# Optimization experiments

Measured on AMD Instinct MI355X. Metric: run time of the kernel, lower is better.

The kernel has to match this reference:

```python
import jax, jax.numpy as jnp
import numpy as np

H = 128  # LSTM units

def setup_inputs() -> dict:
    key = jax.random.key(0)
    ks = jax.random.split(key, 4)
    B, T, F = 16384, 28, 28
    x = jax.random.normal(ks[0], (B, T, F), dtype=jnp.float32)
    W = jax.random.normal(ks[1], (F, 4 * H), dtype=jnp.float32) * (1.0 / np.sqrt(F))
    U = jax.random.normal(ks[2], (H, 4 * H), dtype=jnp.float32) * (1.0 / np.sqrt(H))
    b = jnp.zeros((4 * H,), dtype=jnp.float32)
    Wd = jax.random.normal(ks[3], (H, 10), dtype=jnp.float32) * (1.0 / np.sqrt(H))
    bd = jnp.zeros((10,), dtype=jnp.float32)
    return {"x": x, "W": W, "U": U, "b": b, "Wd": Wd, "bd": bd}

def reference(x, W, U, b, Wd, bd):
    B = x.shape[0]
    # Precompute input projection for all timesteps: [B, T, 4H]
    xW = jnp.einsum('btf,fg->btg', x, W) + b
    xW_t = jnp.swapaxes(xW, 0, 1)  # [T, B, 4H] for scan

    def step(carry, xw):
        h, c = carry
        z = xw + h @ U  # [B, 4H]
        i, f, g, o = jnp.split(z, 4, axis=-1)  # Keras gate order: i, f, c, o
        i = jax.nn.sigmoid(i)
        f = jax.nn.sigmoid(f)
        g = jax.nn.relu(g)          # activation='relu' on cell candidate
        o = jax.nn.sigmoid(o)
        c_new = f * c + i * g
        h_new = o * jax.nn.relu(c_new)  # activation='relu' on cell state
        return (h_new, c_new), None

    h0 = jnp.zeros((B, H), dtype=x.dtype)
    c0 = jnp.zeros((B, H), dtype=x.dtype)
    (h_final, _), _ = jax.lax.scan(step, (h0, c0), xW_t)
    logits = h_final @ Wd + bd
    return jax.nn.softmax(logits, axis=-1)
```

## Files before the change

kernel.cpp:

```cpp
#include <hip/hip_runtime.h>
#include <math.h>

constexpr int LH = 128;
constexpr int LG = 512;
constexpr int LT = 28;
constexpr int LF = 28;
constexpr int NS = 16;
constexpr int NTH = 512;
constexpr int NREC = 8 * 4 * 5;

typedef short bf16x8 __attribute__((ext_vector_type(8)));
typedef float f32x4  __attribute__((ext_vector_type(4)));

__device__ __forceinline__ unsigned short rne_bf16(float f) {
    unsigned u = __builtin_bit_cast(unsigned, f);
    u += 0x7FFFu + ((u >> 16) & 1u);
    return (unsigned short)(u >> 16);
}
__device__ __forceinline__ float bf16_to_f(unsigned short v) {
    return __builtin_bit_cast(float, (unsigned)v << 16);
}
__device__ __forceinline__ float fsigmoid(float v) {
    return __builtin_amdgcn_rcpf(1.0f + __expf(-v));
}

__device__ __forceinline__ int h_idx(int row, int g, int w2) {
    return row * LH + (((g ^ (row & 15)) << 3) + w2);
}

__global__ __launch_bounds__(256) void pack_frags(
    const float* __restrict__ W, const float* __restrict__ U,
    const float* __restrict__ b, unsigned short* __restrict__ ws)
{
    const int gid = blockIdx.x * 256 + threadIdx.x;
    if (gid >= NREC * 64) return;
    const int lane = gid & 63;
    const int rec  = gid >> 6;
    const int kk   = rec % 5;
    const int wti  = rec / 5;
    const int ti   = wti & 3;
    const int w    = wti >> 2;
    const int r16  = lane & 15;
    const int quad = lane >> 4;
    const int col  = 128 * ti + 16 * w + r16;

    unsigned short v[8];
#pragma unroll
    for (int e = 0; e < 8; ++e) {
        float f;
        if (kk < 4) {
            f = U[(kk * 32 + quad * 8 + e) * LG + col];
        } else {
            const int k = quad * 8 + e;
            f = (k < LF) ? W[k * LG + col] : (k == LF ? b[col] : 0.0f);
        }
        v[e] = rne_bf16(f);
    }
    unsigned short* dst = ws + (size_t)gid * 8;
#pragma unroll
    for (int e = 0; e < 8; ++e) dst[e] = v[e];
}

__global__ __launch_bounds__(NTH, 4) void lstm_mfma(
    const float* __restrict__ x,
    const bf16x8* __restrict__ frag,
    const float* __restrict__ Wd,
    const float* __restrict__ bd,
    float* __restrict__ out)
{
    __shared__ unsigned short xfrag[LT][4][16][8];
    __shared__ unsigned short h_sh[2][NS * LH];
    __shared__ bf16x8 wlds[8 * 4 * 64];
    __shared__ float logit_lds[NS][10];

    const int tid  = threadIdx.x;
    const int wave = tid >> 6;
    const int lane = tid & 63;
    const int r16  = lane & 15;
    const int quad = lane >> 4;
    const long s0  = (long)blockIdx.x * NS;

    bf16x8 Uf[4][4];
#pragma unroll
    for (int ti = 0; ti < 4; ++ti)
#pragma unroll
        for (int kk = 0; kk < 4; ++kk)
            Uf[ti][kk] = frag[((wave * 4 + ti) * 5 + kk) * 64 + lane];

    for (int i = tid; i < 8 * 4 * 64; i += NTH)
        wlds[i] = frag[((i >> 6) * 5 + 4) * 64 + (i & 63)];

    for (int i = tid; i < NS * LH; i += NTH) h_sh[0][i] = 0;

#pragma unroll 1
    for (int i = tid; i < LT * NS * 32; i += NTH) {
        const int fpad = i & 31;
        const int s    = (i >> 5) & 15;
        const int t    = i >> 9;
        float v;
        if (fpad < LF)       v = x[(s0 + s) * (LT * LF) + t * LF + fpad];
        else if (fpad == LF) v = 1.0f;
        else                 v = 0.0f;
        xfrag[t][fpad >> 3][s][fpad & 7] = rne_bf16(v);
    }

    float cre[4];
#pragma unroll
    for (int e = 0; e < 4; ++e) cre[e] = 0.0f;

    int cur = 0;
#pragma unroll 1
    for (int t = 0; t < LT; ++t) {
        __syncthreads();

        f32x4 acc[4];
#pragma unroll
        for (int ti = 0; ti < 4; ++ti)
            acc[ti] = f32x4{0.0f, 0.0f, 0.0f, 0.0f};

        {
            const bf16x8 xa = *reinterpret_cast<const bf16x8*>(
                &xfrag[t][quad][r16][0]);
#pragma unroll
            for (int ti = 0; ti < 4; ++ti) {
                const bf16x8 wf = wlds[(wave * 4 + ti) * 64 + lane];
                acc[ti] = __builtin_amdgcn_mfma_f32_16x16x32_bf16(
                    xa, wf, acc[ti], 0, 0, 0);
            }
        }

#pragma unroll
        for (int kk = 0; kk < 4; ++kk) {
            const bf16x8 h0 = *reinterpret_cast<const bf16x8*>(
                &h_sh[cur][h_idx(r16, kk * 4 + quad, 0)]);
#pragma unroll
            for (int ti = 0; ti < 4; ++ti)
                acc[ti] = __builtin_amdgcn_mfma_f32_16x16x32_bf16(
                    h0, Uf[ti][kk], acc[ti], 0, 0, 0);
        }

        const int gW = 2 * wave + (r16 >> 3);
        const int w2 = r16 & 7;
#pragma unroll
        for (int e = 0; e < 4; ++e) {
            const float ig = fsigmoid(acc[0][e]);
            const float fg = fsigmoid(acc[1][e]);
            const float gg = fmaxf(acc[2][e], 0.0f);
            const float og = fsigmoid(acc[3][e]);
            const float cn = fg * cre[e] + ig * gg;
            cre[e] = cn;
            const float hv = og * fmaxf(cn, 0.0f);
            h_sh[cur ^ 1][h_idx(quad * 4 + e, gW, w2)] = rne_bf16(hv);
        }
        cur ^= 1;
    }

    __syncthreads();

    if (tid < NS * 10) {
        const int s   = tid / 10;
        const int cls = tid - s * 10;
        float a = bd[cls];
        for (int k = 0; k < LH; ++k) {
            const float hv = bf16_to_f(
                h_sh[cur][s * LH + ((((k >> 3) ^ s) << 3) + (k & 7))]);
            a += hv * Wd[k * 10 + cls];
        }
        logit_lds[s][cls] = a;
    }
    __syncthreads();

    if (tid < NS) {
        const int s = tid;
        float m = logit_lds[s][0];
#pragma unroll
        for (int q = 1; q < 10; ++q) m = fmaxf(m, logit_lds[s][q]);
        float e[10], sum = 0.0f;
#pragma unroll
        for (int q = 0; q < 10; ++q) {
            e[q] = expf(logit_lds[s][q] - m);
            sum += e[q];
        }
        const float inv = __builtin_amdgcn_rcpf(sum);
#pragma unroll
        for (int q = 0; q < 10; ++q)
            out[(s0 + s) * 10 + q] = e[q] * inv;
    }
}

extern "C" void kernel_launch(void* const* d_in, const int* in_sizes, int n_in,
                              void* d_out, int out_size, void* d_ws, size_t ws_size,
                              hipStream_t stream) {
    const float* x  = (const float*)d_in[0];
    const float* W  = (const float*)d_in[1];
    const float* U  = (const float*)d_in[2];
    const float* b  = (const float*)d_in[3];
    const float* Wd = (const float*)d_in[4];
    const float* bd = (const float*)d_in[5];
    float* out = (float*)d_out;

    const int B = in_sizes[0] / (LT * LF);
    const int blocks = B / NS;

    pack_frags<<<(NREC * 64 + 255) / 256, 256, 0, stream>>>(
        W, U, b, (unsigned short*)d_ws);
    lstm_mfma<<<blocks, NTH, 0, stream>>>(
        x, (const bf16x8*)d_ws, Wd, bd, out);
}
```

Measured before the change: 108.3 us.

## Process 64 sequences per block with register-resident W fragments

Each block now handles 64 sequences instead of 16, so every wave loops over four 16-row tiles while reusing the same U and W fragments held in registers. The W fragments move from LDS into registers, which removes the per-step LDS reads for them. Occupancy is pinned to 2 waves per EU and bf16 conversion uses the HIP intrinsic. The intent is to amortise weight loads and barriers over more rows, at the cost of 4x fewer blocks and higher register and LDS use.

```diff
diff --git a/kernel.cpp b/kernel.cpp
--- a/kernel.cpp
+++ b/kernel.cpp
@@ -1,11 +1,12 @@
 #include <hip/hip_runtime.h>
+#include <hip/hip_bf16.h>
 #include <math.h>
 
 constexpr int LH = 128;
 constexpr int LG = 512;
 constexpr int LT = 28;
 constexpr int LF = 28;
-constexpr int NS = 16;
+constexpr int NS = 64;
 constexpr int NTH = 512;
 constexpr int NREC = 8 * 4 * 5;
 
@@ -16,6 +17,10 @@
     unsigned u = __builtin_bit_cast(unsigned, f);
     u += 0x7FFFu + ((u >> 16) & 1u);
     return (unsigned short)(u >> 16);
+}
+__device__ __forceinline__ unsigned short hw_bf16(float f) {
+    __hip_bfloat16 h = __float2bfloat16(f);
+    return __builtin_bit_cast(unsigned short, h);
 }
 __device__ __forceinline__ float bf16_to_f(unsigned short v) {
     return __builtin_bit_cast(float, (unsigned)v << 16);
@@ -61,16 +66,16 @@
     for (int e = 0; e < 8; ++e) dst[e] = v[e];
 }
 
-__global__ __launch_bounds__(NTH, 4) void lstm_mfma(
+__global__ __attribute__((amdgpu_waves_per_eu(2, 2))) __launch_bounds__(NTH)
+void lstm_mfma(
     const float* __restrict__ x,
     const bf16x8* __restrict__ frag,
     const float* __restrict__ Wd,
     const float* __restrict__ bd,
     float* __restrict__ out)
 {
-    __shared__ unsigned short xfrag[LT][4][16][8];
+    __shared__ unsigned short xfrag[LT][4][4][16][8];
     __shared__ unsigned short h_sh[2][NS * LH];
-    __shared__ bf16x8 wlds[8 * 4 * 64];
     __shared__ float logit_lds[NS][10];
 
     const int tid  = threadIdx.x;
@@ -81,89 +86,85 @@
     const long s0  = (long)blockIdx.x * NS;
 
     bf16x8 Uf[4][4];
-#pragma unroll
-    for (int ti = 0; ti < 4; ++ti)
+    bf16x8 Wf[4];
+#pragma unroll
+    for (int ti = 0; ti < 4; ++ti) {
 #pragma unroll
         for (int kk = 0; kk < 4; ++kk)
             Uf[ti][kk] = frag[((wave * 4 + ti) * 5 + kk) * 64 + lane];
-
-    for (int i = tid; i < 8 * 4 * 64; i += NTH)
-        wlds[i] = frag[((i >> 6) * 5 + 4) * 64 + (i & 63)];
+        Wf[ti] = frag[((wave * 4 + ti) * 5 + 4) * 64 + lane];
+    }
 
     for (int i = tid; i < NS * LH; i += NTH) h_sh[0][i] = 0;
 
-#pragma unroll 1
+#pragma unroll 8
     for (int i = tid; i < LT * NS * 32; i += NTH) {
         const int fpad = i & 31;
-        const int s    = (i >> 5) & 15;
-        const int t    = i >> 9;
+        const int s    = (i >> 5) & 63;
+        const int t    = i >> 11;
         float v;
         if (fpad < LF)       v = x[(s0 + s) * (LT * LF) + t * LF + fpad];
         else if (fpad == LF) v = 1.0f;
         else                 v = 0.0f;
-        xfrag[t][fpad >> 3][s][fpad & 7] = rne_bf16(v);
-    }
-
-    float cre[4];
-#pragma unroll
-    for (int e = 0; e < 4; ++e) cre[e] = 0.0f;
+        xfrag[t][s >> 4][fpad >> 3][s & 15][fpad & 7] = hw_bf16(v);
+    }
+
+    float cre[4][4];
+#pragma unroll
+    for (int rt = 0; rt < 4; ++rt)
+#pragma unroll
+        for (int e = 0; e < 4; ++e) cre[rt][e] = 0.0f;
+
+    const f32x4 Z4 = f32x4{0.0f, 0.0f, 0.0f, 0.0f};
+    const int gW = 2 * wave + (r16 >> 3);
+    const int w2 = r16 & 7;
 
     int cur = 0;
 #pragma unroll 1
     for (int t = 0; t < LT; ++t) {
         __syncthreads();
 
-        f32x4 acc[4];
-#pragma unroll
-        for (int ti = 0; ti < 4; ++ti)
-            acc[ti] = f32x4{0.0f, 0.0f, 0.0f, 0.0f};
-
-        {
+#pragma unroll
+        for (int rt = 0; rt < 4; ++rt) {
             const bf16x8 xa = *reinterpret_cast<const bf16x8*>(
-                &xfrag[t][quad][r16][0]);
-#pragma unroll
-            for (int ti = 0; ti < 4; ++ti) {
-                const bf16x8 wf = wlds[(wave * 4 + ti) * 64 + lane];
-                acc[ti] = __builtin_amdgcn_mfma_f32_16x16x32_bf16(
-                    xa, wf, acc[ti], 0, 0, 0);
+                &xfrag[t][rt][quad][r16][0]);
+            f32x4 a0 = __builtin_amdgcn_mfma_f32_16x16x32_bf16(xa, Wf[0], Z4, 0, 0, 0);
+            f32x4 a1 = __builtin_amdgcn_mfma_f32_16x16x32_bf16(xa, Wf[1], Z4, 0, 0, 0);
+            f32x4 a2 = __builtin_amdgcn_mfma_f32_16x16x32_bf16(xa, Wf[2], Z4, 0, 0, 0);
+            f32x4 a3 = __builtin_amdgcn_mfma_f32_16x16x32_bf16(xa, Wf[3], Z4, 0, 0, 0);
+#pragma unroll
+            for (int kk = 0; kk < 4; ++kk) {
+                const bf16x8 h0 = *reinterpret_cast<const bf16x8*>(
+                    &h_sh[cur][h_idx(rt * 16 + r16, kk * 4 + quad, 0)]);
+                a0 = __builtin_amdgcn_mfma_f32_16x16x32_bf16(h0, Uf[0][kk], a0, 0, 0, 0);
+                a1 = __builtin_amdgcn_mfma_f32_16x16x32_bf16(h0, Uf[1][kk], a1, 0, 0, 0);
+                a2 = __builtin_amdgcn_mfma_f32_16x16x32_bf16(h0, Uf[2][kk], a2, 0, 0, 0);
+                a3 = __builtin_amdgcn_mfma_f32_16x16x32_bf16(h0, Uf[3][kk], a3, 0, 0, 0);
             }
-        }
-
-#pragma unroll
-        for (int kk = 0; kk < 4; ++kk) {
-            const bf16x8 h0 = *reinterpret_cast<const bf16x8*>(
-                &h_sh[cur][h_idx(r16, kk * 4 + quad, 0)]);
-#pragma unroll
-            for (int ti = 0; ti < 4; ++ti)
-                acc[ti] = __builtin_amdgcn_mfma_f32_16x16x32_bf16(
-                    h0, Uf[ti][kk], acc[ti], 0, 0, 0);
-        }
-
-        const int gW = 2 * wave + (r16 >> 3);
-        const int w2 = r16 & 7;
-#pragma unroll
-        for (int e = 0; e < 4; ++e) {
-            const float ig = fsigmoid(acc[0][e]);
-            const float fg = fsigmoid(acc[1][e]);
-            const float gg = fmaxf(acc[2][e], 0.0f);
-            const float og = fsigmoid(acc[3][e]);
-            const float cn = fg * cre[e] + ig * gg;
-            cre[e] = cn;
-            const float hv = og * fmaxf(cn, 0.0f);
-            h_sh[cur ^ 1][h_idx(quad * 4 + e, gW, w2)] = rne_bf16(hv);
+#pragma unroll
+            for (int e = 0; e < 4; ++e) {
+                const float ig = fsigmoid(a0[e]);
+                const float fg = fsigmoid(a1[e]);
+                const float gg = fmaxf(a2[e], 0.0f);
+                const float og = fsigmoid(a3[e]);
+                const float cn = fg * cre[rt][e] + ig * gg;
+                cre[rt][e] = cn;
+                const float hv = og * fmaxf(cn, 0.0f);
+                h_sh[cur ^ 1][h_idx(rt * 16 + quad * 4 + e, gW, w2)] = hw_bf16(hv);
+            }
         }
         cur ^= 1;
     }
 
     __syncthreads();
 
-    if (tid < NS * 10) {
-        const int s   = tid / 10;
-        const int cls = tid - s * 10;
+    for (int i = tid; i < NS * 10; i += NTH) {
+        const int s   = i / 10;
+        const int cls = i - s * 10;
         float a = bd[cls];
         for (int k = 0; k < LH; ++k) {
             const float hv = bf16_to_f(
-                h_sh[cur][s * LH + ((((k >> 3) ^ s) << 3) + (k & 7))]);
+                h_sh[cur][s * LH + ((((k >> 3) ^ (s & 15)) << 3) + (k & 7))]);
             a += hv * Wd[k * 10 + cls];
         }
         logit_lds[s][cls] = a;
```

Result: slower. 121.5 us (+12.2%).
